# Optimization experiments

Measured on AMD Instinct MI355X. Metric: run time of the kernel, lower is better.

## Reference

```python
import jax, jax.numpy as jnp
import numpy as np

N = 8192
E_DIM = 256
HID = 256
OUT = 128
N_PRED = 2_000_000


def setup_inputs() -> dict:
    key = jax.random.key(0)
    ks = jax.random.split(key, 6)
    node_indices = jnp.arange(N, dtype=jnp.int64) if jax.config.jax_enable_x64 else jnp.arange(N, dtype=jnp.int32)
    attn_matrix = jax.random.normal(ks[0], (N, N), dtype=jnp.float32)
    edge_label_index = jax.random.randint(ks[1], (2, N_PRED), 0, N)
    emb = jax.random.normal(ks[2], (N, E_DIM), dtype=jnp.float32) * 0.05
    W1 = jax.random.normal(ks[3], (E_DIM, HID), dtype=jnp.float32) * (1.0 / np.sqrt(E_DIM))
    b1 = jnp.zeros((HID,), dtype=jnp.float32)
    W2 = jax.random.normal(ks[4], (HID, OUT), dtype=jnp.float32) * (1.0 / np.sqrt(HID))
    b2 = jnp.zeros((OUT,), dtype=jnp.float32)
    return {"node_indices": node_indices, "attn_matrix": attn_matrix,
            "edge_label_index": edge_label_index, "emb": emb,
            "W1": W1, "b1": b1, "W2": W2, "b2": b2}


def reference(node_indices, attn_matrix, edge_label_index, emb, W1, b1, W2, b2):
    # dense_to_sparse of an (almost surely) all-nonzero dense matrix keeps all
    # N^2 edges (incl. diagonal), so no extra self-loops are added by gcn_norm.
    w = jax.nn.relu(attn_matrix)                       # edge weights after F.relu
    deg = w.sum(axis=0)                                # deg[j] = sum_i w[i,j] (scatter on col)
    dis = jnp.where(deg > 0, jax.lax.rsqrt(deg), 0.0)  # deg^{-1/2}, inf -> 0
    a_norm = dis[:, None] * w * dis[None, :]           # norm_ij = d_i^-1/2 w_ij d_j^-1/2

    x = emb[node_indices]                              # embedding lookup [N, E_DIM]
    # GCNConv: aggregate transformed features at target (col): out = A_norm^T @ (x W) + b
    h = jax.nn.relu(a_norm.T @ (x @ W1) + b1)          # [N, HID]
    z = a_norm.T @ (h @ W2) + b2                       # [N, OUT]

    # decode: dot product between endpoint embeddings
    scores = jnp.einsum('ed,ed->e', z[edge_label_index[0]], z[edge_label_index[1]])
    return scores
```

## Files before the change

kernel.cpp:

```cpp
#include <hip/hip_runtime.h>

typedef _Float16 half8  __attribute__((ext_vector_type(8)));
typedef _Float16 half4v __attribute__((ext_vector_type(4)));
typedef _Float16 half2v __attribute__((ext_vector_type(2)));
typedef float    floatx4 __attribute__((ext_vector_type(4)));
typedef float    f4v     __attribute__((ext_vector_type(4)));

#define NND 8192
#define PA  40
#define PT  136

__device__ __forceinline__ int swzk(int m, int k) { return k ^ (((m >> 3) & 3) << 3); }

__global__ __launch_bounds__(256) void k_degT(const float* __restrict__ A,
                                              _Float16* __restrict__ Wh,
                                              float* __restrict__ deg) {
    __shared__ _Float16 T[128 * PT];
    __shared__ float sdeg[8 * 128];
    int t  = threadIdx.x;
    int j0 = blockIdx.x * 128, i0 = blockIdx.y * 128;
    int c = t & 31;
    int g = t >> 5;

    f4v s = {0.f, 0.f, 0.f, 0.f};
    #pragma unroll
    for (int p = 0; p < 2; ++p) {
        int rb = 64 * p + 8 * g;
        f4v v[8];
        #pragma unroll
        for (int rr = 0; rr < 8; ++rr)
            v[rr] = *(const f4v*)(A + (size_t)(i0 + rb + rr) * NND + j0 + 4 * c);
        #pragma unroll
        for (int rr = 0; rr < 8; ++rr)
            #pragma unroll
            for (int u = 0; u < 4; ++u) v[rr][u] = fmaxf(v[rr][u], 0.f);
        #pragma unroll
        for (int u = 0; u < 4; ++u) {
            half8 hv;
            #pragma unroll
            for (int rr = 0; rr < 8; ++rr) { hv[rr] = (_Float16)v[rr][u]; s[u] += v[rr][u]; }
            *(half8*)(&T[(4 * c + u) * PT + rb]) = hv;
        }
    }
    *(f4v*)(&sdeg[g * 128 + 4 * c]) = s;
    __syncthreads();

    if (t < 128) {
        float d = 0.f;
        #pragma unroll
        for (int g2 = 0; g2 < 8; ++g2) d += sdeg[g2 * 128 + t];
        atomicAdd(&deg[j0 + t], d);
    }

    #pragma unroll
    for (int p = 0; p < 8; ++p) {
        int j  = 16 * p + (t >> 4);
        int ic = (t & 15) * 8;
        half8 hv = *(const half8*)(&T[j * PT + ic]);
        *(half8*)(Wh + (size_t)(j0 + j) * NND + i0 + ic) = hv;
    }
}

__global__ __launch_bounds__(256) void k_dis(const float* __restrict__ deg, float* __restrict__ dis) {
    int j = blockIdx.x * 256 + threadIdx.x;
    float d = deg[j];
    dis[j] = d > 0.f ? 1.f / sqrtf(d) : 0.f;
}

template <typename AT>
__global__ __launch_bounds__(256) void k_mm_small(
    const AT* __restrict__ Abase, const int* __restrict__ gather,
    const float* __restrict__ B, int NB,
    _Float16* __restrict__ outT, const float* __restrict__ dis, float out_scale) {

    __shared__ _Float16 As[128 * PA];
    __shared__ _Float16 Bs[64 * PA];

    int t  = threadIdx.x;
    int i0 = blockIdx.x * 128;
    int n0 = blockIdx.y * 64;

    int am = t & 127, akh = t >> 7;
    int row = i0 + am;
    if (gather) row = gather[row];
    const AT* arow = Abase + (size_t)row * 256;

    int tp = t & 15, kp = t >> 4;

    int lane = t & 63, w = t >> 6;
    int wm = w & 1, wn = w >> 1;
    int lm = lane & 15, q = lane >> 4;

    floatx4 acc[4][2];
    #pragma unroll
    for (int a = 0; a < 4; ++a)
        #pragma unroll
        for (int b = 0; b < 2; ++b) acc[a][b] = (floatx4){0.f, 0.f, 0.f, 0.f};

    for (int ks = 0; ks < 8; ++ks) {
        int c0 = ks * 32;

        half8 av[2];
        if constexpr (sizeof(AT) == 4) {
            #pragma unroll
            for (int cc = 0; cc < 2; ++cc) {
                f4v v0 = *(const f4v*)(arow + c0 + akh * 16 + cc * 8);
                f4v v1 = *(const f4v*)(arow + c0 + akh * 16 + cc * 8 + 4);
                half8 hv;
                #pragma unroll
                for (int e = 0; e < 4; ++e) {
                    hv[e]     = (_Float16)(16.f * v0[e]);
                    hv[4 + e] = (_Float16)(16.f * v1[e]);
                }
                av[cc] = hv;
            }
        } else {
            av[0] = *(const half8*)(arow + c0 + akh * 16);
            av[1] = *(const half8*)(arow + c0 + akh * 16 + 8);
        }

        const float* bp = B + (size_t)(c0 + 2 * kp) * NB + n0 + 4 * tp;
        f4v r0 = *(const f4v*)bp;
        f4v r1 = *(const f4v*)(bp + NB);

        __syncthreads();
        #pragma unroll
        for (int cc = 0; cc < 2; ++cc) {
            int k = akh * 16 + cc * 8;
            *(half8*)(&As[am * PA + swzk(am, k)]) = av[cc];
        }
        #pragma unroll
        for (int u = 0; u < 4; ++u) {
            int n = 4 * tp + u;
            half2v p = {(_Float16)r0[u], (_Float16)r1[u]};
            *(half2v*)(&Bs[n * PA + swzk(n, 2 * kp)]) = p;
        }
        __syncthreads();

        half8 af[4], bf[2];
        #pragma unroll
        for (int mt = 0; mt < 4; ++mt) {
            int m = wm * 64 + mt * 16 + lm;
            af[mt] = *(const half8*)(&As[m * PA + swzk(m, q * 8)]);
        }
        #pragma unroll
        for (int nt = 0; nt < 2; ++nt) {
            int n = wn * 32 + nt * 16 + lm;
            bf[nt] = *(const half8*)(&Bs[n * PA + swzk(n, q * 8)]);
        }
        #pragma unroll
        for (int mt = 0; mt < 4; ++mt)
            #pragma unroll
            for (int nt = 0; nt < 2; ++nt)
                acc[mt][nt] = __builtin_amdgcn_mfma_f32_16x16x32_f16(af[mt], bf[nt], acc[mt][nt], 0, 0, 0);
    }

    #pragma unroll
    for (int mt = 0; mt < 4; ++mt) {
        int ib = i0 + wm * 64 + mt * 16 + q * 4;
        #pragma unroll
        for (int nt = 0; nt < 2; ++nt) {
            int n = n0 + wn * 32 + nt * 16 + lm;
            #pragma unroll
            for (int r = 0; r < 4; ++r) {
                float v = acc[mt][nt][r] * dis[ib + r] * out_scale;
                outT[(size_t)n * NND + ib + r] = (_Float16)v;
            }
        }
    }
}

template <int BN>
__global__ __launch_bounds__(256, 2) void k_mm_big(
    const _Float16* __restrict__ Wh, const _Float16* __restrict__ Bt, float* __restrict__ Cp) {

    constexpr int NT = BN / 32;
    __shared__ _Float16 As[128 * PA];
    __shared__ _Float16 Bs[BN * PA];

    int t = threadIdx.x;
    int j0 = blockIdx.x * 128;
    int i_begin = blockIdx.z * 1024;
    float* C = Cp + (size_t)blockIdx.z * NND * BN;

    int ar = t & 127, akh = t >> 7;
    int lane = t & 63, w = t >> 6;
    int wm = w & 1, wn = w >> 1;
    int lm = lane & 15, q = lane >> 4;

    floatx4 acc[4][NT];
    #pragma unroll
    for (int a = 0; a < 4; ++a)
        #pragma unroll
        for (int b = 0; b < NT; ++b) acc[a][b] = (floatx4){0.f, 0.f, 0.f, 0.f};

    for (int ks = 0; ks < 32; ++ks) {
        int ib = i_begin + ks * 32;

        const _Float16* asrc = Wh + (size_t)(j0 + ar) * NND + ib + 16 * akh;
        half8 av[2];
        av[0] = *(const half8*)(asrc);
        av[1] = *(const half8*)(asrc + 8);

        half8 bv[(BN == 256) ? 4 : 2];
        if constexpr (BN == 256) {
            const _Float16* src = Bt + (size_t)t * NND + ib;
            #pragma unroll
            for (int c = 0; c < 4; ++c) bv[c] = *(const half8*)(src + 8 * c);
        } else {
            int n = t & 127, kh = t >> 7;
            const _Float16* src = Bt + (size_t)n * NND + ib + 16 * kh;
            #pragma unroll
            for (int c = 0; c < 2; ++c) bv[c] = *(const half8*)(src + 8 * c);
        }

        __syncthreads();
        #pragma unroll
        for (int c = 0; c < 2; ++c) {
            int k = 16 * akh + 8 * c;
            *(half8*)(&As[ar * PA + swzk(ar, k)]) = av[c];
        }
        if constexpr (BN == 256) {
            #pragma unroll
            for (int c = 0; c < 4; ++c)
                *(half8*)(&Bs[t * PA + swzk(t, 8 * c)]) = bv[c];
        } else {
            int n = t & 127, kh = t >> 7;
            #pragma unroll
            for (int c = 0; c < 2; ++c) {
                int k = 16 * kh + 8 * c;
                *(half8*)(&Bs[n * PA + swzk(n, k)]) = bv[c];
            }
        }
        __syncthreads();

        half8 af[4], bf[NT];
        #pragma unroll
        for (int mt = 0; mt < 4; ++mt) {
            int m = wm * 64 + mt * 16 + lm;
            af[mt] = *(const half8*)(&As[m * PA + swzk(m, q * 8)]);
        }
        #pragma unroll
        for (int nt = 0; nt < NT; ++nt) {
            int n = wn * (BN / 2) + nt * 16 + lm;
            bf[nt] = *(const half8*)(&Bs[n * PA + swzk(n, q * 8)]);
        }
        #pragma unroll
        for (int mt = 0; mt < 4; ++mt)
            #pragma unroll
            for (int nt = 0; nt < NT; ++nt)
                acc[mt][nt] = __builtin_amdgcn_mfma_f32_16x16x32_f16(af[mt], bf[nt], acc[mt][nt], 0, 0, 0);
    }

    #pragma unroll
    for (int mt = 0; mt < 4; ++mt) {
        int rb = j0 + wm * 64 + mt * 16 + q * 4;
        #pragma unroll
        for (int nt = 0; nt < NT; ++nt) {
            int col = wn * (BN / 2) + nt * 16 + lm;
            #pragma unroll
            for (int r = 0; r < 4; ++r)
                C[(size_t)(rb + r) * BN + col] = acc[mt][nt][r];
        }
    }
}

template <int NSH, bool RELU>
__global__ __launch_bounds__(256) void k_finalize(const float* __restrict__ Cp, const float* __restrict__ dis,
                                                  const float* __restrict__ bias, _Float16* __restrict__ out) {
    int idx = blockIdx.x * 256 + threadIdx.x;
    float v = 0.f;
    #pragma unroll
    for (int z = 0; z < 8; ++z) v += Cp[(size_t)z * (NND << NSH) + idx];
    int j = idx >> NSH;
    int n = idx & ((1 << NSH) - 1);
    v = v * (1.f / 1024.f) * dis[j] + bias[n];
    if (RELU) v = fmaxf(v, 0.f);
    out[idx] = (_Float16)(v * 64.f);
}

__global__ __launch_bounds__(256) void k_edges(const _Float16* __restrict__ zh, const int* __restrict__ ei,
                                               float* __restrict__ out, int npred) {
    int g = (blockIdx.x * 256 + threadIdx.x) >> 4;
    int l = threadIdx.x & 15;
    if (g >= npred) return;
    int a = ei[g], b = ei[npred + g];
    half8 za = *(const half8*)(zh + (size_t)a * 128 + l * 8);
    half8 zb = *(const half8*)(zh + (size_t)b * 128 + l * 8);
    float s = 0.f;
    #pragma unroll
    for (int e = 0; e < 8; ++e) s += (float)za[e] * (float)zb[e];
    s += __shfl_xor(s, 1);
    s += __shfl_xor(s, 2);
    s += __shfl_xor(s, 4);
    s += __shfl_xor(s, 8);
    if (l == 0) out[g] = s * (1.f / 4096.f);
}

extern "C" void kernel_launch(void* const* d_in, const int* in_sizes, int n_in,
                              void* d_out, int out_size, void* d_ws, size_t ws_size,
                              hipStream_t stream) {
    const int*   nodes = (const int*)d_in[0];
    const float* attn  = (const float*)d_in[1];
    const int*   eidx  = (const int*)d_in[2];
    const float* emb   = (const float*)d_in[3];
    const float* W1    = (const float*)d_in[4];
    const float* b1    = (const float*)d_in[5];
    const float* W2    = (const float*)d_in[6];
    const float* b2    = (const float*)d_in[7];
    float* out = (float*)d_out;
    int npred = in_sizes[2] / 2;

    char* ws = (char*)d_ws;
    float*    deg = (float*)(ws);
    float*    dis = (float*)(ws + 0x8000);
    _Float16* Wh  = (_Float16*)(ws + 0x10000);
    float*    C1p = (float*)(ws + 0x8010000);
    float*    C2p = (float*)(ws + 0xC010000);
    _Float16* M1p = (_Float16*)(ws + 0xE010000);
    _Float16* h   = (_Float16*)(ws + 0xE410000);
    _Float16* M2p = (_Float16*)(ws + 0xE810000);
    _Float16* zh  = (_Float16*)(ws + 0xEA10000);

    hipMemsetAsync(deg, 0, 8192 * sizeof(float), stream);

    k_degT<<<dim3(64, 64), 256, 0, stream>>>(attn, Wh, deg);
    k_dis<<<32, 256, 0, stream>>>(deg, dis);

    k_mm_small<float><<<dim3(64, 4), 256, 0, stream>>>(emb, nodes, W1, 256, M1p, dis, 64.f);
    k_mm_big<256><<<dim3(64, 1, 8), 256, 0, stream>>>(Wh, M1p, C1p);
    k_finalize<8, true><<<8192, 256, 0, stream>>>(C1p, dis, b1, h);
    k_mm_small<_Float16><<<dim3(64, 2), 256, 0, stream>>>(h, nullptr, W2, 128, M2p, dis, 16.f);
    k_mm_big<128><<<dim3(64, 1, 8), 256, 0, stream>>>(Wh, M2p, C2p);
    k_finalize<7, false><<<4096, 256, 0, stream>>>(C2p, dis, b2, zh);

    k_edges<<<(npred + 15) / 16, 256, 0, stream>>>(zh, eidx, out, npred);
}
```

Measured before the change: 645.7 us.

## Use direct global-to-LDS loads and 128x128 tiles in big GEMM

Replaces the register-staged global loads and swizzled LDS stores in k_mm_big with global_load_lds direct copies into unpadded LDS tiles, and fixes the N tile to 128, adding a grid y dimension to cover BN=256. This removes the VGPR round trip and the extra store instructions, and doubles the block count for the first GEMM. In exchange, the swizzle is dropped, so LDS fragment reads may hit bank conflicts. The loop is still single-buffered, and the A tile is now loaded twice in the BN=256 case.

```diff
diff --git a/kernel.cpp b/kernel.cpp
--- a/kernel.cpp
+++ b/kernel.cpp
@@ -11,6 +11,10 @@
 #define PT  136
 
 __device__ __forceinline__ int swzk(int m, int k) { return k ^ (((m >> 3) & 3) << 3); }
+
+#define GLOAD16(gp, lp) __builtin_amdgcn_global_load_lds(                        \
+    (const __attribute__((address_space(1))) void*)(gp),                         \
+    (__attribute__((address_space(3))) void*)(lp), 16, 0, 0)
 
 __global__ __launch_bounds__(256) void k_degT(const float* __restrict__ A,
                                               _Float16* __restrict__ Wh,
@@ -171,93 +175,73 @@
 }
 
 template <int BN>
-__global__ __launch_bounds__(256, 2) void k_mm_big(
+__global__ __launch_bounds__(256) void k_mm_big(
     const _Float16* __restrict__ Wh, const _Float16* __restrict__ Bt, float* __restrict__ Cp) {
 
-    constexpr int NT = BN / 32;
-    __shared__ _Float16 As[128 * PA];
-    __shared__ _Float16 Bs[BN * PA];
+    __shared__ __align__(16) _Float16 As[128 * 32];
+    __shared__ __align__(16) _Float16 Bs[128 * 32];
 
     int t = threadIdx.x;
     int j0 = blockIdx.x * 128;
-    int i_begin = blockIdx.z * 1024;
-    float* C = Cp + (size_t)blockIdx.z * NND * BN;
-
-    int ar = t & 127, akh = t >> 7;
+    int n0 = blockIdx.y * 128;
+    size_t i_begin = (size_t)blockIdx.z * 1024;
+    float* C = Cp + (size_t)blockIdx.z * (size_t)NND * BN;
+
     int lane = t & 63, w = t >> 6;
     int wm = w & 1, wn = w >> 1;
     int lm = lane & 15, q = lane >> 4;
 
-    floatx4 acc[4][NT];
+    int srow = lane >> 2;
+    int scol = (lane & 3) * 8;
+    const _Float16* aS0 = Wh + (size_t)(j0 + w * 16 + srow) * NND + i_begin + scol;
+    const _Float16* aS1 = aS0 + (size_t)64 * NND;
+    const _Float16* bS0 = Bt + (size_t)(n0 + w * 16 + srow) * NND + i_begin + scol;
+    const _Float16* bS1 = bS0 + (size_t)64 * NND;
+
+    char* aL0 = (char*)As + w * 1024;
+    char* aL1 = (char*)As + (4 + w) * 1024;
+    char* bL0 = (char*)Bs + w * 1024;
+    char* bL1 = (char*)Bs + (4 + w) * 1024;
+
+    floatx4 acc[4][4];
     #pragma unroll
     for (int a = 0; a < 4; ++a)
         #pragma unroll
-        for (int b = 0; b < NT; ++b) acc[a][b] = (floatx4){0.f, 0.f, 0.f, 0.f};
+        for (int b = 0; b < 4; ++b) acc[a][b] = (floatx4){0.f, 0.f, 0.f, 0.f};
 
     for (int ks = 0; ks < 32; ++ks) {
-        int ib = i_begin + ks * 32;
-
-        const _Float16* asrc = Wh + (size_t)(j0 + ar) * NND + ib + 16 * akh;
-        half8 av[2];
-        av[0] = *(const half8*)(asrc);
-        av[1] = *(const half8*)(asrc + 8);
-
-        half8 bv[(BN == 256) ? 4 : 2];
-        if constexpr (BN == 256) {
-            const _Float16* src = Bt + (size_t)t * NND + ib;
-            #pragma unroll
-            for (int c = 0; c < 4; ++c) bv[c] = *(const half8*)(src + 8 * c);
-        } else {
-            int n = t & 127, kh = t >> 7;
-            const _Float16* src = Bt + (size_t)n * NND + ib + 16 * kh;
-            #pragma unroll
-            for (int c = 0; c < 2; ++c) bv[c] = *(const half8*)(src + 8 * c);
-        }
-
+        int ko = ks * 32;
+        GLOAD16(aS0 + ko, aL0);
+        GLOAD16(aS1 + ko, aL1);
+        GLOAD16(bS0 + ko, bL0);
+        GLOAD16(bS1 + ko, bL1);
         __syncthreads();
-        #pragma unroll
-        for (int c = 0; c < 2; ++c) {
-            int k = 16 * akh + 8 * c;
-            *(half8*)(&As[ar * PA + swzk(ar, k)]) = av[c];
-        }
-        if constexpr (BN == 256) {
-            #pragma unroll
-            for (int c = 0; c < 4; ++c)
-                *(half8*)(&Bs[t * PA + swzk(t, 8 * c)]) = bv[c];
-        } else {
-            int n = t & 127, kh = t >> 7;
-            #pragma unroll
-            for (int c = 0; c < 2; ++c) {
-                int k = 16 * kh + 8 * c;
-                *(half8*)(&Bs[n * PA + swzk(n, k)]) = bv[c];
-            }
-        }
-        __syncthreads();
-
-        half8 af[4], bf[NT];
+
+        half8 af[4], bf[4];
         #pragma unroll
         for (int mt = 0; mt < 4; ++mt) {
             int m = wm * 64 + mt * 16 + lm;
-            af[mt] = *(const half8*)(&As[m * PA + swzk(m, q * 8)]);
-        }
-        #pragma unroll
-        for (int nt = 0; nt < NT; ++nt) {
-            int n = wn * (BN / 2) + nt * 16 + lm;
-            bf[nt] = *(const half8*)(&Bs[n * PA + swzk(n, q * 8)]);
+            af[mt] = *(const half8*)(&As[m * 32 + q * 8]);
+        }
+        #pragma unroll
+        for (int nt = 0; nt < 4; ++nt) {
+            int n = wn * 64 + nt * 16 + lm;
+            bf[nt] = *(const half8*)(&Bs[n * 32 + q * 8]);
         }
         #pragma unroll
         for (int mt = 0; mt < 4; ++mt)
             #pragma unroll
-            for (int nt = 0; nt < NT; ++nt)
+            for (int nt = 0; nt < 4; ++nt)
                 acc[mt][nt] = __builtin_amdgcn_mfma_f32_16x16x32_f16(af[mt], bf[nt], acc[mt][nt], 0, 0, 0);
+        __syncthreads();
     }
 
     #pragma unroll
     for (int mt = 0; mt < 4; ++mt) {
         int rb = j0 + wm * 64 + mt * 16 + q * 4;
         #pragma unroll
-        for (int nt = 0; nt < NT; ++nt) {
-            int col = wn * (BN / 2) + nt * 16 + lm;
+        for (int nt = 0; nt < 4; ++nt) {
+            int col = n0 + wn * 64 + nt * 16 + lm;
             #pragma unroll
             for (int r = 0; r < 4; ++r)
                 C[(size_t)(rb + r) * BN + col] = acc[mt][nt][r];
@@ -328,7 +312,7 @@
     k_dis<<<32, 256, 0, stream>>>(deg, dis);
 
     k_mm_small<float><<<dim3(64, 4), 256, 0, stream>>>(emb, nodes, W1, 256, M1p, dis, 64.f);
-    k_mm_big<256><<<dim3(64, 1, 8), 256, 0, stream>>>(Wh, M1p, C1p);
+    k_mm_big<256><<<dim3(64, 2, 8), 256, 0, stream>>>(Wh, M1p, C1p);
     k_finalize<8, true><<<8192, 256, 0, stream>>>(C1p, dis, b1, h);
     k_mm_small<_Float16><<<dim3(64, 2), 256, 0, stream>>>(h, nullptr, W2, 128, M2p, dis, 16.f);
     k_mm_big<128><<<dim3(64, 1, 8), 256, 0, stream>>>(Wh, M2p, C2p);
```

After: 642.3 us. No clear change (-0.5%).
